# Optimization experiments

Hardware: AMD Instinct MI355X
Metric: run time of the kernel (lower is better)

## Reference

```python
import jax, jax.numpy as jnp
import numpy as np

N, E = 20000, 320000
IN, H, C = 1024, 8, 64
HC = H * C
EDGE_DIM = 16
NUM_GRAPHS = 8
LEAKY_SLOPE = 0.2
LN_EPS = 1e-5


def setup_inputs() -> dict:
    key = jax.random.key(0)
    ks = jax.random.split(key, 12)
    s = 0.05
    return {
        "x": jax.random.normal(ks[0], (N, IN), jnp.float32),
        "edge_attr": jax.random.normal(ks[1], (E, EDGE_DIM), jnp.float32),
        "edge_index": jax.random.randint(ks[2], (2, E), 0, N, dtype=jnp.int64),
        "batch": jnp.sort(jax.random.randint(ks[3], (N,), 0, NUM_GRAPHS, dtype=jnp.int64)),
        "W_src": jax.random.normal(ks[4], (IN, HC), jnp.float32) * s,
        "W_dst": jax.random.normal(ks[5], (IN, HC), jnp.float32) * s,
        "att_src": jax.random.normal(ks[6], (H, C), jnp.float32) * s,
        "att_dst": jax.random.normal(ks[7], (H, C), jnp.float32) * s,
        "bias": jnp.zeros((HC,), jnp.float32),
        "ln_gamma": jnp.ones((HC,), jnp.float32),
        "ln_beta": jnp.zeros((HC,), jnp.float32),
        "prelu_a": jnp.full((HC,), 0.25, jnp.float32),
    }


def reference(x, edge_attr, edge_index, batch, W_src, W_dst, att_src, att_dst,
              bias, ln_gamma, ln_beta, prelu_a):
    # Eval mode: node/edge feature dropout and attention dropout are identity.
    # with_edge == 'N': edge_attr is unused by the conv.
    n = x.shape[0]
    src, dst = edge_index[0], edge_index[1]

    xs = (x @ W_src).reshape(n, H, C)   # source-side projections
    xd = (x @ W_dst).reshape(n, H, C)   # dest-side projections
    a_src = jnp.einsum('nhc,hc->nh', xs, att_src)
    a_dst = jnp.einsum('nhc,hc->nh', xd, att_dst)

    # edge scores + softmax over incoming edges of each destination node
    e = jax.nn.leaky_relu(a_src[src] + a_dst[dst], LEAKY_SLOPE)  # [E,H]
    m = jax.ops.segment_max(e, dst, num_segments=n)              # [N,H]
    m = jax.lax.stop_gradient(jnp.where(jnp.isfinite(m), m, 0.0))
    ex = jnp.exp(e - m[dst])
    denom = jax.ops.segment_sum(ex, dst, num_segments=n)
    alpha = ex / (denom[dst] + 1e-16)                            # [E,H]

    msg = alpha[:, :, None] * xs[src]                            # [E,H,C]
    out = jax.ops.segment_sum(msg, dst, num_segments=n).reshape(n, HC) + bias

    # norm_type == 'layer': the per-graph boolean-mask loop applies LayerNorm
    # row-wise; with sorted batch ids this equals a single LayerNorm over all
    # nodes (LayerNorm has no cross-row statistics).
    mu = jnp.mean(out, axis=-1, keepdims=True)
    var = jnp.mean(jnp.square(out - mu), axis=-1, keepdims=True)
    y = (out - mu) * jax.lax.rsqrt(var + LN_EPS) * ln_gamma + ln_beta

    # PReLU with per-channel slope
    return jnp.where(y >= 0, y, prelu_a * y)
```

## Files before the change

### kernel.cpp

```cpp
#include <hip/hip_runtime.h>
#include <hip/hip_bf16.h>

#define N_NODES 20000
#define N_EDGES 320000
#define IN_DIM  1024
#define H_HEADS 8
#define C_CH    64
#define HC      512
#define LEAKY   0.2f
#define LN_EPS  1e-5f

#define BCOLS 576

typedef short bf16x8 __attribute__((ext_vector_type(8)));
typedef float f32x4  __attribute__((ext_vector_type(4)));

__device__ __forceinline__ unsigned short f2bf(float f) {
    union { float f; unsigned int u; } c; c.f = f;
    unsigned int u = c.u;
    unsigned int r = (u + 0x7fffu + ((u >> 16) & 1u)) >> 16;
    return (unsigned short)r;
}
__device__ __forceinline__ float bf2f(unsigned int h) {
    union { unsigned int u; float f; } c; c.u = h << 16; return c.f;
}
__device__ __forceinline__ unsigned int cvtpk(float lo, float hi) {
    unsigned int r;
    asm("v_cvt_pk_bf16_f32 %0, %1, %2" : "=v"(r) : "v"(lo), "v"(hi));
    return r;
}
__device__ __forceinline__ void gload_lds16(const void* g, void* l) {
    __builtin_amdgcn_global_load_lds(
        (const __attribute__((address_space(1))) unsigned int*)g,
        (__attribute__((address_space(3))) unsigned int*)l, 16, 0, 0);
}

#define DEG_BLOCKS 1250

__global__ __launch_bounds__(256) void deg_hist(
        const int* __restrict__ ei, int* __restrict__ deg) {
    int e = blockIdx.x * 256 + threadIdx.x;
    atomicAdd(&deg[ei[N_EDGES + e]], 1);
}

__global__ void prep_w_scan(const float* __restrict__ Wsrc,
                            const float* __restrict__ Wdst,
                            const float* __restrict__ att_src,
                            const float* __restrict__ att_dst,
                            short* __restrict__ wbT,
                            const int* __restrict__ deg,
                            int* __restrict__ off,
                            int* __restrict__ cursor) {
    int t = threadIdx.x;

    if (blockIdx.x == IN_DIM) {
        __shared__ int wtot[2];
        int lane = t & 63, w = t >> 6;
        const int4* deg4 = (const int4*)deg;
        int s = 0;
        if (t < 125) {
            #pragma unroll
            for (int j = 0; j < 40; ++j) {
                int4 u = deg4[t * 40 + j];
                s += u.x + u.y + u.z + u.w;
            }
        }
        int v = s;
        #pragma unroll
        for (int o = 1; o < 64; o <<= 1) {
            int u = __shfl_up(v, o);
            if (lane >= o) v += u;
        }
        if (lane == 63) wtot[w] = v;
        __syncthreads();
        int add = (w == 1) ? wtot[0] : 0;
        int run = add + v - s;
        if (t < 125) {
            int4* off4 = (int4*)off;
            int4* cur4 = (int4*)cursor;
            #pragma unroll
            for (int j = 0; j < 40; ++j) {
                int4 u = deg4[t * 40 + j];
                int4 o_;
                o_.x = run;
                o_.y = o_.x + u.x;
                o_.z = o_.y + u.y;
                o_.w = o_.z + u.z;
                off4[t * 40 + j] = o_;
                cur4[t * 40 + j] = o_;
                run = o_.w + u.w;
            }
            if (t == 124) off[N_NODES] = run;
        }
        return;
    }

    int k = blockIdx.x;
    float4 v = *(const float4*)(Wsrc + (size_t)k * HC + t * 4);
    wbT[(size_t)(t * 4 + 0) * IN_DIM + k] = (short)f2bf(v.x);
    wbT[(size_t)(t * 4 + 1) * IN_DIM + k] = (short)f2bf(v.y);
    wbT[(size_t)(t * 4 + 2) * IN_DIM + k] = (short)f2bf(v.z);
    wbT[(size_t)(t * 4 + 3) * IN_DIM + k] = (short)f2bf(v.w);
    if (t < 16) {
        int h = t & 7;
        const float* W   = (t < 8) ? Wsrc : Wdst;
        const float* att = (t < 8) ? att_src : att_dst;
        float s = 0.f;
        #pragma unroll
        for (int c = 0; c < C_CH; ++c)
            s += W[(size_t)k * HC + h * C_CH + c] * att[h * C_CH + c];
        wbT[(size_t)(512 + t) * IN_DIM + k] = (short)f2bf(s);
    } else if (t < 64) {
        wbT[(size_t)(512 + t) * IN_DIM + k] = 0;
    }
}

#define BM 64
#define BN 96
#define BK 64
#define NCOLT (BCOLS / BN)
#define NROWT ((N_NODES + BM - 1) / BM)
#define NWG (NCOLT * NROWT)
#define KSTEPS (IN_DIM / BK)
#define A_SLOTS (BM * BK / 8)
#define B_SLOTS (BN * BK / 8)

__global__ __launch_bounds__(256) void gemm_scatter(
        const float* __restrict__ x,
        const short* __restrict__ wbT,
        short* __restrict__ xsb,
        float* __restrict__ a_srcv,
        float* __restrict__ a_dstv,
        const int* __restrict__ ei,
        int* __restrict__ cursor,
        int* __restrict__ csr_src) {
    __shared__ short As[2][A_SLOTS * 8];
    __shared__ short Bs[2][B_SLOTS * 8];

    int t = threadIdx.x;

    if (blockIdx.x >= NWG) {
        int e = (blockIdx.x - NWG) * 256 + t;
        int d = ei[N_EDGES + e];
        int idx = atomicAdd(&cursor[d], 1);
        csr_src[idx] = ei[e];
        return;
    }

    int orig = blockIdx.x;
    const int q = NWG >> 3, r = NWG & 7;
    int xcd  = orig & 7;
    int wgid = (xcd < r ? xcd * (q + 1) : r * (q + 1) + (xcd - r) * q) + (orig >> 3);
    int col0 = (wgid % NCOLT) * BN;
    int row0 = (wgid / NCOLT) * BM;

    int lane = t & 63;
    int w    = t >> 6;
    int lr   = lane & 15;
    int lg   = lane >> 4;
    int sw   = lr & 7;
    int wr   = (w >> 1) * 32;
    int wc   = (w & 1) * 48;

    const float* a_base[2];
    #pragma unroll
    for (int i = 0; i < 2; ++i) {
        int s  = t + 256 * i;
        int m  = s >> 3;
        int kc = (s & 7) ^ (m & 7);
        int gm = row0 + m;
        if (gm >= N_NODES) gm = N_NODES - 1;
        a_base[i] = x + (size_t)gm * IN_DIM + kc * 8;
    }
    const short* b_base[3];
    #pragma unroll
    for (int i = 0; i < 3; ++i) {
        int s  = t + 256 * i;
        int c  = s >> 3;
        int kc = (s & 7) ^ (c & 7);
        b_base[i] = wbT + (size_t)(col0 + c) * IN_DIM + kc * 8;
    }

    f32x4 acc[2][3] = {};

#define A_WRITE(buf, fa0, fb0, fa1, fb1)                                      \
    do {                                                                      \
        uint4 r0, r1;                                                         \
        r0.x = cvtpk(fa0.x, fa0.y);  r0.y = cvtpk(fa0.z, fa0.w);              \
        r0.z = cvtpk(fb0.x, fb0.y);  r0.w = cvtpk(fb0.z, fb0.w);              \
        r1.x = cvtpk(fa1.x, fa1.y);  r1.y = cvtpk(fa1.z, fa1.w);              \
        r1.z = cvtpk(fb1.x, fb1.y);  r1.w = cvtpk(fb1.z, fb1.w);              \
        *(uint4*)(&As[buf][(t      ) * 8]) = r0;                              \
        *(uint4*)(&As[buf][(t + 256) * 8]) = r1;                              \
    } while (0)

#define COMPUTE(buf)                                                          \
    do {                                                                      \
        _Pragma("unroll")                                                     \
        for (int ks = 0; ks < 2; ++ks) {                                      \
            int kc  = ks * 4 + lg;                                            \
            int kca = kc ^ sw;                                                \
            bf16x8 af[2], bfr[3];                                             \
            _Pragma("unroll")                                                 \
            for (int mi = 0; mi < 2; ++mi)                                    \
                af[mi] = *(const bf16x8*)(&As[buf][((wr + mi * 16 + lr) * 8 + kca) * 8]); \
            _Pragma("unroll")                                                 \
            for (int ni = 0; ni < 3; ++ni)                                    \
                bfr[ni] = *(const bf16x8*)(&Bs[buf][((wc + ni * 16 + lr) * 8 + kca) * 8]); \
            __builtin_amdgcn_s_setprio(1);                                    \
            _Pragma("unroll")                                                 \
            for (int mi = 0; mi < 2; ++mi)                                    \
                _Pragma("unroll")                                             \
                for (int ni = 0; ni < 3; ++ni)                                \
                    acc[mi][ni] = __builtin_amdgcn_mfma_f32_16x16x32_bf16(    \
                        af[mi], bfr[ni], acc[mi][ni], 0, 0, 0);               \
            __builtin_amdgcn_s_setprio(0);                                    \
        }                                                                     \
    } while (0)

    {
        float4 fa0 = *(const float4*)(a_base[0]);
        float4 fb0 = *(const float4*)(a_base[0] + 4);
        float4 fa1 = *(const float4*)(a_base[1]);
        float4 fb1 = *(const float4*)(a_base[1] + 4);
        #pragma unroll
        for (int i = 0; i < 3; ++i)
            gload_lds16(b_base[i], &Bs[0][(t + 256 * i) * 8]);
        A_WRITE(0, fa0, fb0, fa1, fb1);
        asm volatile("s_waitcnt vmcnt(0) lgkmcnt(0)" ::: "memory");
        __builtin_amdgcn_s_barrier();
    }

    int cur = 0;
    for (int step = 0; step < KSTEPS; ++step) {
        float4 fa0, fb0, fa1, fb1;
        if (step + 1 < KSTEPS) {
            int k1 = (step + 1) * BK;
            fa0 = *(const float4*)(a_base[0] + k1);
            fb0 = *(const float4*)(a_base[0] + k1 + 4);
            fa1 = *(const float4*)(a_base[1] + k1);
            fb1 = *(const float4*)(a_base[1] + k1 + 4);
            #pragma unroll
            for (int i = 0; i < 3; ++i)
                gload_lds16(b_base[i] + k1, &Bs[cur ^ 1][(t + 256 * i) * 8]);
        }

        COMPUTE(cur);

        if (step + 1 < KSTEPS)
            A_WRITE(cur ^ 1, fa0, fb0, fa1, fb1);

        asm volatile("s_waitcnt vmcnt(0) lgkmcnt(0)" ::: "memory");
        __builtin_amdgcn_s_barrier();
        cur ^= 1;
    }
#undef A_WRITE
#undef COMPUTE

    #pragma unroll
    for (int mi = 0; mi < 2; ++mi) {
        #pragma unroll
        for (int rr = 0; rr < 4; ++rr) {
            int row = row0 + wr + mi * 16 + lg * 4 + rr;
            if (row >= N_NODES) continue;
            #pragma unroll
            for (int ni = 0; ni < 3; ++ni) {
                int col = col0 + wc + ni * 16 + lr;
                float v = acc[mi][ni][rr];
                if (col < 512)      xsb[(size_t)row * HC + col] = (short)f2bf(v);
                else if (col < 520) a_srcv[(size_t)row * 8 + (col - 512)] = v;
                else if (col < 528) a_dstv[(size_t)row * 8 + (col - 520)] = v;
            }
        }
    }
}

__global__ __launch_bounds__(256) void aggregate_ln(
        const int* __restrict__ off,
        const int* __restrict__ csr_src,
        const float* __restrict__ a_srcv,
        const float* __restrict__ a_dstv,
        const short* __restrict__ xsb,
        const float* __restrict__ bias,
        const float* __restrict__ gamma,
        const float* __restrict__ beta,
        const float* __restrict__ prelu_a,
        float* __restrict__ out) {
    int lane = threadIdx.x & 63;
    int n    = blockIdx.x * 4 + (threadIdx.x >> 6);
    int ch0  = lane * 8;
    int h    = lane >> 3;

    int start = off[n], end = off[n + 1];
    float ad  = a_dstv[(size_t)n * 8 + h];

    float acc[8] = {};
    float wsum = 0.f;

    int i = start;
    for (; i + 1 < end; i += 2) {
        int s0 = __builtin_amdgcn_readfirstlane(csr_src[i]);
        int s1 = __builtin_amdgcn_readfirstlane(csr_src[i + 1]);
        float sc0 = a_srcv[(size_t)s0 * 8 + h] + ad;
        float sc1 = a_srcv[(size_t)s1 * 8 + h] + ad;
        uint4 u0 = *(const uint4*)(xsb + (size_t)s0 * HC + ch0);
        uint4 u1 = *(const uint4*)(xsb + (size_t)s1 * HC + ch0);
        sc0 = (sc0 >= 0.f) ? sc0 : LEAKY * sc0;
        sc1 = (sc1 >= 0.f) ? sc1 : LEAKY * sc1;
        float w0 = __expf(sc0);
        float w1 = __expf(sc1);
        acc[0] = fmaf(w0, bf2f(u0.x & 0xffffu), acc[0]);
        acc[1] = fmaf(w0, bf2f(u0.x >> 16),     acc[1]);
        acc[2] = fmaf(w0, bf2f(u0.y & 0xffffu), acc[2]);
        acc[3] = fmaf(w0, bf2f(u0.y >> 16),     acc[3]);
        acc[4] = fmaf(w0, bf2f(u0.z & 0xffffu), acc[4]);
        acc[5] = fmaf(w0, bf2f(u0.z >> 16),     acc[5]);
        acc[6] = fmaf(w0, bf2f(u0.w & 0xffffu), acc[6]);
        acc[7] = fmaf(w0, bf2f(u0.w >> 16),     acc[7]);
        acc[0] = fmaf(w1, bf2f(u1.x & 0xffffu), acc[0]);
        acc[1] = fmaf(w1, bf2f(u1.x >> 16),     acc[1]);
        acc[2] = fmaf(w1, bf2f(u1.y & 0xffffu), acc[2]);
        acc[3] = fmaf(w1, bf2f(u1.y >> 16),     acc[3]);
        acc[4] = fmaf(w1, bf2f(u1.z & 0xffffu), acc[4]);
        acc[5] = fmaf(w1, bf2f(u1.z >> 16),     acc[5]);
        acc[6] = fmaf(w1, bf2f(u1.w & 0xffffu), acc[6]);
        acc[7] = fmaf(w1, bf2f(u1.w >> 16),     acc[7]);
        wsum += w0 + w1;
    }
    if (i < end) {
        int s0 = __builtin_amdgcn_readfirstlane(csr_src[i]);
        float sc0 = a_srcv[(size_t)s0 * 8 + h] + ad;
        uint4 u0 = *(const uint4*)(xsb + (size_t)s0 * HC + ch0);
        sc0 = (sc0 >= 0.f) ? sc0 : LEAKY * sc0;
        float w0 = __expf(sc0);
        acc[0] = fmaf(w0, bf2f(u0.x & 0xffffu), acc[0]);
        acc[1] = fmaf(w0, bf2f(u0.x >> 16),     acc[1]);
        acc[2] = fmaf(w0, bf2f(u0.y & 0xffffu), acc[2]);
        acc[3] = fmaf(w0, bf2f(u0.y >> 16),     acc[3]);
        acc[4] = fmaf(w0, bf2f(u0.z & 0xffffu), acc[4]);
        acc[5] = fmaf(w0, bf2f(u0.z >> 16),     acc[5]);
        acc[6] = fmaf(w0, bf2f(u0.w & 0xffffu), acc[6]);
        acc[7] = fmaf(w0, bf2f(u0.w >> 16),     acc[7]);
        wsum += w0;
    }

    float inv = 1.f / (wsum + 1e-16f);
    float4 b0 = *(const float4*)(bias + ch0);
    float4 b1 = *(const float4*)(bias + ch0 + 4);
    float v8[8];
    float psum = 0.f, psq = 0.f;
    const float bb[8] = {b0.x, b0.y, b0.z, b0.w, b1.x, b1.y, b1.z, b1.w};
    #pragma unroll
    for (int j = 0; j < 8; ++j) {
        v8[j] = acc[j] * inv + bb[j];
        psum += v8[j];
        psq  += v8[j] * v8[j];
    }
    #pragma unroll
    for (int o = 32; o > 0; o >>= 1) {
        psum += __shfl_xor(psum, o);
        psq  += __shfl_xor(psq, o);
    }
    float mu   = psum * (1.f / (float)HC);
    float var  = psq * (1.f / (float)HC) - mu * mu;
    float rstd = rsqrtf(var + LN_EPS);

    float4 g0 = *(const float4*)(gamma + ch0);
    float4 g1 = *(const float4*)(gamma + ch0 + 4);
    float4 e0 = *(const float4*)(beta + ch0);
    float4 e1 = *(const float4*)(beta + ch0 + 4);
    float4 p0 = *(const float4*)(prelu_a + ch0);
    float4 p1 = *(const float4*)(prelu_a + ch0 + 4);
    const float gg[8] = {g0.x, g0.y, g0.z, g0.w, g1.x, g1.y, g1.z, g1.w};
    const float ee[8] = {e0.x, e0.y, e0.z, e0.w, e1.x, e1.y, e1.z, e1.w};
    const float pp[8] = {p0.x, p0.y, p0.z, p0.w, p1.x, p1.y, p1.z, p1.w};
    float y[8];
    #pragma unroll
    for (int j = 0; j < 8; ++j) {
        float v = (v8[j] - mu) * rstd * gg[j] + ee[j];
        y[j] = (v >= 0.f) ? v : pp[j] * v;
    }
    float4* o4 = (float4*)(out + (size_t)n * HC + ch0);
    o4[0] = make_float4(y[0], y[1], y[2], y[3]);
    o4[1] = make_float4(y[4], y[5], y[6], y[7]);
}

extern "C" void kernel_launch(void* const* d_in, const int* in_sizes, int n_in,
                              void* d_out, int out_size, void* d_ws, size_t ws_size,
                              hipStream_t stream) {
    const float* x        = (const float*)d_in[0];
    const int*   ei       = (const int*)d_in[2];
    const float* Wsrc     = (const float*)d_in[4];
    const float* Wdst     = (const float*)d_in[5];
    const float* att_src  = (const float*)d_in[6];
    const float* att_dst  = (const float*)d_in[7];
    const float* bias     = (const float*)d_in[8];
    const float* gamma    = (const float*)d_in[9];
    const float* beta     = (const float*)d_in[10];
    const float* prelu_a  = (const float*)d_in[11];
    float* out            = (float*)d_out;

    char*  ws = (char*)d_ws;
    size_t o  = 0;
    auto alloc = [&](size_t bytes) -> void* {
        void* p = ws + o;
        o += (bytes + 255) & ~(size_t)255;
        return p;
    };
    short* wbT     = (short*)alloc(sizeof(short) * BCOLS * IN_DIM);
    short* xsb     = (short*)alloc(sizeof(short) * (size_t)N_NODES * HC);
    float* a_srcv  = (float*)alloc(sizeof(float) * N_NODES * 8);
    float* a_dstv  = (float*)alloc(sizeof(float) * N_NODES * 8);
    int*   deg     = (int*)alloc(sizeof(int) * N_NODES);
    int*   off     = (int*)alloc(sizeof(int) * (N_NODES + 1));
    int*   cursor  = (int*)alloc(sizeof(int) * N_NODES);
    int*   csr_src = (int*)alloc(sizeof(int) * N_EDGES);

    hipMemsetAsync(deg, 0, sizeof(int) * N_NODES, stream);

    deg_hist<<<DEG_BLOCKS, 256, 0, stream>>>(ei, deg);

    prep_w_scan<<<IN_DIM + 1, 128, 0, stream>>>(Wsrc, Wdst, att_src, att_dst,
                                                wbT, deg, off, cursor);

    gemm_scatter<<<NWG + DEG_BLOCKS, 256, 0, stream>>>(
        x, wbT, xsb, a_srcv, a_dstv, ei, cursor, csr_src);

    aggregate_ln<<<N_NODES / 4, 256, 0, stream>>>(
        off, csr_src, a_srcv, a_dstv, xsb, bias, gamma, beta, prelu_a, out);
}
```

Measured before the change: 147.6 us.

## Deepen GEMM prefetch pipeline with two-step A register lookahead and partial vmcnt waits

Restructures the GEMM main loop so global loads of A fp32 tiles are issued two K-steps ahead into a double-buffered register array, while B tiles stream to LDS one step ahead. Uses partial s_waitcnt vmcnt counts instead of full drains, so the in-flight loads for later steps stay outstanding while the current tile is computed. The loop is fully unrolled and adds a second barrier per step. This raises register pressure and depends on the exact count of in-flight memory operations for correctness.

```diff
diff --git a/kernel.cpp b/kernel.cpp
--- a/kernel.cpp
+++ b/kernel.cpp
@@ -124,6 +124,8 @@
 #define KSTEPS (IN_DIM / BK)
 #define A_SLOTS (BM * BK / 8)
 #define B_SLOTS (BN * BK / 8)
+
+#define WAITV(n) asm volatile("s_waitcnt vmcnt(" #n ")" ::: "memory")
 
 __global__ __launch_bounds__(256) void gemm_scatter(
         const float* __restrict__ x,
@@ -218,41 +220,51 @@
         }                                                                     \
     } while (0)
 
+    float4 AR[2][4];
+
     {
-        float4 fa0 = *(const float4*)(a_base[0]);
-        float4 fb0 = *(const float4*)(a_base[0] + 4);
-        float4 fa1 = *(const float4*)(a_base[1]);
-        float4 fb1 = *(const float4*)(a_base[1] + 4);
+        float4 p0 = *(const float4*)(a_base[0]);
+        float4 p1 = *(const float4*)(a_base[0] + 4);
+        float4 p2 = *(const float4*)(a_base[1]);
+        float4 p3 = *(const float4*)(a_base[1] + 4);
+        AR[1][0] = *(const float4*)(a_base[0] + BK);
+        AR[1][1] = *(const float4*)(a_base[0] + BK + 4);
+        AR[1][2] = *(const float4*)(a_base[1] + BK);
+        AR[1][3] = *(const float4*)(a_base[1] + BK + 4);
         #pragma unroll
         for (int i = 0; i < 3; ++i)
             gload_lds16(b_base[i], &Bs[0][(t + 256 * i) * 8]);
-        A_WRITE(0, fa0, fb0, fa1, fb1);
-        asm volatile("s_waitcnt vmcnt(0) lgkmcnt(0)" ::: "memory");
-        __builtin_amdgcn_s_barrier();
-    }
-
-    int cur = 0;
-    for (int step = 0; step < KSTEPS; ++step) {
-        float4 fa0, fb0, fa1, fb1;
-        if (step + 1 < KSTEPS) {
-            int k1 = (step + 1) * BK;
-            fa0 = *(const float4*)(a_base[0] + k1);
-            fb0 = *(const float4*)(a_base[0] + k1 + 4);
-            fa1 = *(const float4*)(a_base[1] + k1);
-            fb1 = *(const float4*)(a_base[1] + k1 + 4);
+        A_WRITE(0, p0, p1, p2, p3);
+        asm volatile("s_waitcnt lgkmcnt(0)" ::: "memory");
+    }
+
+    #pragma unroll
+    for (int s = 0; s < KSTEPS; ++s) {
+        if (s + 2 < KSTEPS) {
+            int k2 = (s + 2) * BK;
+            AR[s & 1][0] = *(const float4*)(a_base[0] + k2);
+            AR[s & 1][1] = *(const float4*)(a_base[0] + k2 + 4);
+            AR[s & 1][2] = *(const float4*)(a_base[1] + k2);
+            AR[s & 1][3] = *(const float4*)(a_base[1] + k2 + 4);
+        }
+        if (s + 1 < KSTEPS) {
+            int k1 = (s + 1) * BK;
             #pragma unroll
             for (int i = 0; i < 3; ++i)
-                gload_lds16(b_base[i] + k1, &Bs[cur ^ 1][(t + 256 * i) * 8]);
-        }
-
-        COMPUTE(cur);
-
-        if (step + 1 < KSTEPS)
-            A_WRITE(cur ^ 1, fa0, fb0, fa1, fb1);
-
-        asm volatile("s_waitcnt vmcnt(0) lgkmcnt(0)" ::: "memory");
+                gload_lds16(b_base[i] + k1, &Bs[(s + 1) & 1][(t + 256 * i) * 8]);
+        }
+        if (s + 2 < KSTEPS)      WAITV(7);
+        else if (s + 1 < KSTEPS) WAITV(3);
+        else                     WAITV(0);
         __builtin_amdgcn_s_barrier();
-        cur ^= 1;
+
+        COMPUTE(s & 1);
+
+        if (s + 1 < KSTEPS)
+            A_WRITE((s + 1) & 1, AR[(s + 1) & 1][0], AR[(s + 1) & 1][1],
+                                 AR[(s + 1) & 1][2], AR[(s + 1) & 1][3]);
+        asm volatile("s_waitcnt lgkmcnt(0)" ::: "memory");
+        __builtin_amdgcn_s_barrier();
     }
 #undef A_WRITE
 #undef COMPUTE
```

Result: no change. 148.3 us (+0.5%).
